# Kernel optimization log

Hardware: AMD Instinct MI355X
Metric: run time of the kernel (lower is better)

## Reference

```python
import jax, jax.numpy as jnp
import numpy as np

B, N, D, H = 4, 2048, 512, 8
KD = D // H  # per-head key/value dim = 64
NORM = 1.0 / np.sqrt(KD).astype(np.float32)


def setup_inputs() -> dict:
    key = jax.random.key(0)
    kq, km, k1, k2, k3 = jax.random.split(key, 5)
    s = 1.0 / np.sqrt(D)
    return {
        "queries": jax.random.normal(kq, (B, N, D), dtype=jnp.float32),
        "mask": jax.random.randint(km, (B, N, N), 0, 2).astype(jnp.bool_),
        "Wq": jax.random.normal(k1, (D, D), dtype=jnp.float32) * s,
        "Wk": jax.random.normal(k2, (D, D), dtype=jnp.float32) * s,
        "Wc": jax.random.normal(k3, (D, D), dtype=jnp.float32) * s,
    }


def reference(queries, mask, Wq, Wk, Wc):
    # Self-attention path (keys=None, values=None): V uses key_embed (Wk).
    Q = (queries @ Wq.T).reshape(B, N, H, KD)  # [B,N,H,kd]
    K = (queries @ Wk.T).reshape(B, N, H, KD)
    V = K  # original code: V = key_embed(queries) when values is None
    scores = NORM * jnp.einsum("bqhd,bkhd->bhqk", Q, K)  # [B,H,N,N]
    scores = jnp.where(mask[:, None, :, :], -jnp.inf, scores)
    attn = jax.nn.softmax(scores, axis=-1)
    out = jnp.einsum("bhqk,bkhd->bqhd", attn, V).reshape(B, N, H * KD)
    return out @ Wc.T  # [B,N,D]
```

## Files before the change

kernel.cpp:

```cpp
#include <hip/hip_runtime.h>
#include <hip/hip_bf16.h>
#include <math.h>

#define B_ 4
#define N_ 2048
#define D_ 512
#define H_ 8
#define NORM2_ 0.18033688011112042f

typedef __attribute__((ext_vector_type(8))) short short8;
typedef __attribute__((ext_vector_type(4))) float f32x4;
#define MFMA16(a, b, c) __builtin_amdgcn_mfma_f32_16x16x32_bf16(a, b, c, 0, 0, 0)
#define EXP2(x) __builtin_amdgcn_exp2f(x)

static __device__ __forceinline__ uint32_t pk2(float lo, float hi) {
  __hip_bfloat162 h = __float22bfloat162_rn(make_float2(lo, hi));
  return *(reinterpret_cast<uint32_t*>(&h));
}

static __device__ __forceinline__ void async16(const ushort* lds, const ushort* g) {
  __builtin_amdgcn_global_load_lds(
      (const __attribute__((address_space(1))) uint32_t*)g,
      (__attribute__((address_space(3))) uint32_t*)(ushort*)lds, 16, 0, 0);
}

__global__ __launch_bounds__(256) void prep(const float* __restrict__ q,
                                            const int* __restrict__ mask,
                                            const float* __restrict__ wq,
                                            const float* __restrict__ wk,
                                            const float* __restrict__ wc,
                                            ushort* __restrict__ Xb,
                                            ushort* __restrict__ Wb,
                                            uint32_t* __restrict__ pk) {
  const int bx = blockIdx.x;
  if (bx < 2048) {
    const int lane = threadIdx.x & 63;
    const int wid = ((bx << 8) + threadIdx.x) >> 6;
    for (int i = wid; i < 65536; i += 8192) {
      const int4 m = ((const int4*)mask)[(size_t)i * 64 + lane];
      uint32_t nib = (uint32_t)(m.x != 0) | ((uint32_t)(m.y != 0) << 1) |
                     ((uint32_t)(m.z != 0) << 2) | ((uint32_t)(m.w != 0) << 3);
      nib |= __shfl_xor(nib, 1) << 4;
      nib |= __shfl_xor(nib, 2) << 8;
      nib |= __shfl_xor(nib, 4) << 16;
      if ((lane & 7) == 0) pk[i * 8 + (lane >> 3)] = nib;
    }
  } else if (bx < 3072) {
    const int i = ((bx - 2048) << 8) + threadIdx.x;
    for (int j = i; j < 1048576; j += 262144) {
      const float4 v = ((const float4*)q)[j];
      uint2 o; o.x = pk2(v.x, v.y); o.y = pk2(v.z, v.w);
      ((uint2*)Xb)[j] = o;
    }
  } else {
    const int i = ((bx - 3072) << 8) + threadIdx.x;
    for (int j = i; j < 196608; j += 24576) {
      const int wi = j >> 16, off = j & 65535;
      const float* src = (wi == 0) ? wq : (wi == 1) ? wk : wc;
      const float4 v = ((const float4*)src)[off];
      uint2 o; o.x = pk2(v.x, v.y); o.y = pk2(v.z, v.w);
      ((uint2*)Wb)[j] = o;
    }
  }
}

__global__ __launch_bounds__(256) void merge(const ushort* __restrict__ P0,
                                             const float* __restrict__ l0,
                                             const float* __restrict__ l1,
                                             ushort* __restrict__ Ab) {
  const int j = (blockIdx.x << 8) + threadIdx.x;
  const int h = (j >> 3) & 7;
  const int tok = j >> 6;
  const int b = tok >> 11, n = tok & 2047;
  const int li = ((b * H_ + h) << 11) + n;
  const float inv = 1.f / (l0[li] + l1[li]);
  const uint4 a0 = ((const uint4*)P0)[j];
  const uint4 a1 = ((const uint4*)Ab)[j];
  uint4 o;
  const uint32_t* u0 = (const uint32_t*)&a0;
  const uint32_t* u1 = (const uint32_t*)&a1;
  uint32_t* uo = (uint32_t*)&o;
#pragma unroll
  for (int m = 0; m < 4; ++m) {
    const float lo = __uint_as_float(u0[m] << 16) + __uint_as_float(u1[m] << 16);
    const float hi = __uint_as_float(u0[m] & 0xFFFF0000u) +
                     __uint_as_float(u1[m] & 0xFFFF0000u);
    uo[m] = pk2(lo * inv, hi * inv);
  }
  ((uint4*)Ab)[j] = o;
}

template <int F32OUT>
__global__ __launch_bounds__(256) void gemm128(const ushort* __restrict__ X,
                                               const ushort* __restrict__ W0,
                                               const ushort* __restrict__ W1,
                                               void* __restrict__ C0,
                                               void* __restrict__ C1,
                                               float s0, float s1) {
  const ushort* Wp = (blockIdx.z == 0) ? W0 : W1;
  void* Cp = (blockIdx.z == 0) ? C0 : C1;
  const float sc = (blockIdx.z == 0) ? s0 : s1;
  const int t = threadIdx.x;
  const int w = t >> 6, lane = t & 63, quad = lane >> 4, c = lane & 15;
  const int wm = w & 1, wn = w >> 1;
  const int n0 = blockIdx.x * 128, m0 = blockIdx.y * 128;
  __shared__ __align__(16) ushort Xs[2][128][64];
  __shared__ __align__(16) ushort Ws[2][128][64];
  f32x4 acc[4][4];
#pragma unroll
  for (int i = 0; i < 4; ++i)
#pragma unroll
    for (int j = 0; j < 4; ++j) acc[i][j] = (f32x4){0.f, 0.f, 0.f, 0.f};

#define GSTAGE(bf, k0)                                                        \
  do {                                                                        \
    _Pragma("unroll") for (int g = 0; g < 4; ++g) {                           \
      const int id = w * 256 + g * 64 + lane;                                 \
      const int row = id >> 3, lch = id & 7;                                  \
      const int gch = lch ^ (row & 7);                                        \
      async16(&Xs[bf][row][lch * 8], X + (size_t)(m0 + row) * D_ + (k0) + gch * 8); \
      async16(&Ws[bf][row][lch * 8], Wp + (size_t)(n0 + row) * D_ + (k0) + gch * 8); \
    }                                                                         \
  } while (0)

  GSTAGE(0, 0);
  __syncthreads();
  const int NK = D_ / 64;
  for (int kt = 0; kt < NK; ++kt) {
    const int bf = kt & 1;
    if (kt + 1 < NK) GSTAGE(bf ^ 1, (kt + 1) * 64);
#pragma unroll
    for (int s = 0; s < 2; ++s) {
      short8 af[4], bt[4];
#pragma unroll
      for (int i = 0; i < 4; ++i) {
        const int rA = wn * 64 + i * 16 + c;
        af[i] = *(const short8*)&Ws[bf][rA][(((s * 4 + quad) ^ (rA & 7)) & 7) * 8];
        const int rB = wm * 64 + i * 16 + c;
        bt[i] = *(const short8*)&Xs[bf][rB][(((s * 4 + quad) ^ (rB & 7)) & 7) * 8];
      }
#pragma unroll
      for (int i = 0; i < 4; ++i)
#pragma unroll
        for (int j = 0; j < 4; ++j) acc[i][j] = MFMA16(af[i], bt[j], acc[i][j]);
    }
    if (kt + 1 < NK) __syncthreads();
  }
#undef GSTAGE
#pragma unroll
  for (int i = 0; i < 4; ++i)
#pragma unroll
    for (int j = 0; j < 4; ++j) {
      const size_t off =
          (size_t)(m0 + wm * 64 + j * 16 + c) * D_ + n0 + wn * 64 + i * 16 + quad * 4;
      if (F32OUT) {
        float4 v; v.x = acc[i][j][0]; v.y = acc[i][j][1]; v.z = acc[i][j][2]; v.w = acc[i][j][3];
        *(float4*)((float*)Cp + off) = v;
      } else {
        uint2 uv;
        uv.x = pk2(acc[i][j][0] * sc, acc[i][j][1] * sc);
        uv.y = pk2(acc[i][j][2] * sc, acc[i][j][3] * sc);
        *(uint2*)((ushort*)Cp + off) = uv;
      }
    }
}

__global__ __launch_bounds__(512) void attn_mfma(const ushort* __restrict__ Qb,
                                                 const ushort* __restrict__ Kb,
                                                 const uint32_t* __restrict__ pk,
                                                 ushort* __restrict__ P0,
                                                 ushort* __restrict__ P1,
                                                 float* __restrict__ l0,
                                                 float* __restrict__ l1) {
  const int qt128 = blockIdx.x >> 1, hf = blockIdx.x & 1;
  const int h = blockIdx.y, b = blockIdx.z;
  const int q0 = qt128 * 128;
  const int t = threadIdx.x;
  const int w = t >> 6, lane = t & 63, quad = lane >> 4, c = lane & 15;

  __shared__ __align__(16) ushort Ks[64][64];
  __shared__ __align__(16) uint32_t KtU[64][32];
  __shared__ __align__(16) ushort QP[8][16][72];
  ushort(*Qs)[64] = (ushort(*)[64]) & QP[0][0][0];
  ushort(*Pq)[16][72] = QP;

#pragma unroll
  for (int p = 0; p < 2; ++p) {
    const int id = t + p * 512;
    const int row = id >> 3, lch = id & 7, gch = lch ^ (row & 7);
    async16(&Qs[row][lch * 8], Qb + (size_t)(b * N_ + q0 + row) * D_ + h * 64 + gch * 8);
  }
  __syncthreads();
  const int rq = (w << 4) + c;
  const short8 bq0 = *(const short8*)&Qs[rq][((quad ^ (rq & 7)) & 7) * 8];
  const short8 bq1 = *(const short8*)&Qs[rq][(((4 + quad) ^ (rq & 7)) & 7) * 8];

  short8 vones;
#pragma unroll
  for (int i = 0; i < 8; ++i) vones[i] = (short)0x3F80;

  f32x4 o[4];
#pragma unroll
  for (int i = 0; i < 4; ++i) o[i] = (f32x4){0.f, 0.f, 0.f, 0.f};
  f32x4 o5 = (f32x4){0.f, 0.f, 0.f, 0.f};

  const int kp = t >> 3, ch = t & 7;
  const int r0 = 2 * kp, r1 = r0 + 1;
  const int ksw0 = ((ch ^ (r0 & 7)) & 7) * 8, ksw1 = ((ch ^ (r1 & 7)) & 7) * 8;
  const ushort* kb0 =
      Kb + (size_t)(b * N_ + hf * 1024 + 2 * kp) * D_ + h * 64 + ch * 8;
  const uint32_t* pkq =
      pk + ((size_t)(b * N_ + q0 + (w << 4) + c) << 6) + hf * 32;

  uint4 c0, c1;
  if (t < 256) {
    c0 = *(const uint4*)kb0;
    c1 = *(const uint4*)(kb0 + D_);
  }
  uint2 cm = *(const uint2*)pkq;
  uint4 nx0, nx1; uint2 nxm;

  const int NT = 16;
  for (int kt = 0; kt < NT; ++kt) {
    __syncthreads();
    if (t < 256) {
      *(uint4*)&Ks[r0][ksw0] = c0;
      *(uint4*)&Ks[r1][ksw1] = c1;
      const uint32_t* a0 = (const uint32_t*)&c0;
      const uint32_t* a1 = (const uint32_t*)&c1;
#pragma unroll
      for (int m = 0; m < 4; ++m) {
        const uint32_t lo = __builtin_amdgcn_perm(a1[m], a0[m], 0x05040100);
        const uint32_t hi = __builtin_amdgcn_perm(a1[m], a0[m], 0x07060302);
        const int j0 = 2 * m, j1 = 2 * m + 1;
        KtU[ch * 8 + j0][(kp & 3) | ((((kp >> 2) ^ j0 ^ ch) & 7) << 2)] = lo;
        KtU[ch * 8 + j1][(kp & 3) | ((((kp >> 2) ^ j1 ^ ch) & 7) << 2)] = hi;
      }
    }
    __syncthreads();

    if (kt + 1 < NT) {
      if (t < 256) {
        const ushort* kbn = kb0 + (size_t)(kt + 1) * 64 * D_;
        nx0 = *(const uint4*)kbn;
        nx1 = *(const uint4*)(kbn + D_);
      }
      nxm = *(const uint2*)(pkq + (kt + 1) * 2);
    }

#pragma unroll
    for (int tI = 0; tI < 4; ++tI) {
      const int rk = tI * 16 + c;
      const short8 aK0 = *(const short8*)&Ks[rk][((quad ^ (rk & 7)) & 7) * 8];
      const short8 aK1 = *(const short8*)&Ks[rk][(((4 + quad) ^ (rk & 7)) & 7) * 8];
      f32x4 z = (f32x4){0.f, 0.f, 0.f, 0.f};
      z = MFMA16(aK0, bq0, z);
      z = MFMA16(aK1, bq1, z);
      const uint32_t mw = (tI < 2) ? cm.x : cm.y;
      const int bb = ((tI & 1) << 4) + quad * 4;
      uint32_t pb[4];
#pragma unroll
      for (int r = 0; r < 4; ++r) {
        const float e = EXP2(z[r]);
        pb[r] = ((mw >> (bb + r)) & 1u) ? 0u : __float_as_uint(e);
      }
      const uint32_t pw0 = __builtin_amdgcn_perm(pb[1], pb[0], 0x07060302);
      const uint32_t pw1 = __builtin_amdgcn_perm(pb[3], pb[2], 0x07060302);
      *(uint2*)&Pq[w][c][tI * 16 + quad * 4] = make_uint2(pw0, pw1);
    }

    const short8 bp0 = *(const short8*)&Pq[w][c][quad * 8];
    const short8 bp1 = *(const short8*)&Pq[w][c][32 + quad * 8];
    o5 = MFMA16(vones, bp0, o5);
    o5 = MFMA16(vones, bp1, o5);
#pragma unroll
    for (int dt = 0; dt < 4; ++dt) {
      const int dd = dt * 16 + c;
      const int g = (c & 7) ^ ((2 * dt + (c >> 3)) & 7);
      const short8 aV0 = *(const short8*)&KtU[dd][((quad ^ g) & 7) << 2];
      const short8 aV1 = *(const short8*)&KtU[dd][(((4 + quad) ^ g) & 7) << 2];
      o[dt] = MFMA16(aV0, bp0, o[dt]);
      o[dt] = MFMA16(aV1, bp1, o[dt]);
    }

    if (kt + 1 < NT) {
      if (t < 256) { c0 = nx0; c1 = nx1; }
      cm = nxm;
    }
  }

  ushort* Pp = hf ? P1 : P0;
  float* lp = hf ? l1 : l0;
#pragma unroll
  for (int dt = 0; dt < 4; ++dt) {
    uint2 uv;
    uv.x = pk2(o[dt][0], o[dt][1]);
    uv.y = pk2(o[dt][2], o[dt][3]);
    *(uint2*)(Pp + (size_t)(b * N_ + q0 + (w << 4) + c) * D_ + h * 64 + dt * 16 + quad * 4) = uv;
  }
  if (quad == 0) lp[((b * H_ + h) << 11) + q0 + (w << 4) + c] = o5[0];
}

extern "C" void kernel_launch(void* const* d_in, const int* in_sizes, int n_in,
                              void* d_out, int out_size, void* d_ws, size_t ws_size,
                              hipStream_t stream) {
  const float* queries = (const float*)d_in[0];
  const int* mask = (const int*)d_in[1];
  const float* Wq = (const float*)d_in[2];
  const float* Wk = (const float*)d_in[3];
  const float* Wc = (const float*)d_in[4];
  float* out = (float*)d_out;

  const size_t nTok = (size_t)B_ * N_;
  const size_t nXD = nTok * D_;
  const size_t nW = (size_t)D_ * D_;
  ushort* Xb = (ushort*)d_ws;
  ushort* Wqb = Xb + nXD;
  ushort* Wkb = Wqb + nW;
  ushort* Wcb = Wkb + nW;
  ushort* Qb = Wcb + nW;
  ushort* Kb = Qb + nXD;
  ushort* Ab = Kb + nXD;
  uint32_t* pk = (uint32_t*)(Ab + nXD);
  ushort* P0 = Xb;
  ushort* P1 = Ab;
  float* l0 = (float*)Wqb;
  float* l1 = (float*)Wkb;

  prep<<<3168, 256, 0, stream>>>(queries, mask, Wq, Wk, Wc, Xb, Wqb, pk);
  gemm128<0><<<dim3(D_ / 128, (int)(nTok / 128), 2), 256, 0, stream>>>(
      Xb, Wqb, Wkb, Qb, Kb, NORM2_, 1.0f);
  attn_mfma<<<dim3(32, H_, B_), 512, 0, stream>>>(Qb, Kb, pk, P0, P1, l0, l1);
  merge<<<2048, 256, 0, stream>>>(P0, l0, l1, Ab);
  gemm128<1><<<dim3(D_ / 128, (int)(nTok / 128), 1), 256, 0, stream>>>(
      Ab, Wcb, nullptr, out, nullptr, 1.0f, 1.0f);
}
```

Baseline: 207.4 us.

## Fuse split-KV merge into output GEMM and use 512-thread GEMM blocks

Removes the separate merge kernel. The output projection GEMM now loads both partial attention outputs and the row sums, normalizes and sums them in registers, and writes the bf16 result into shared memory as its A operand. It also moves both GEMMs from 256 to 512 threads per block, with each wave computing a 64x32 tile instead of 64x64. This saves a kernel launch and a full round-trip of the merged activation through global memory. In exchange, the X operand is loaded synchronously into registers rather than by async copy, and each wave does less MFMA work per LDS load.

```diff
diff --git a/kernel.cpp b/kernel.cpp
--- a/kernel.cpp
+++ b/kernel.cpp
@@ -64,63 +64,36 @@
   }
 }
 
-__global__ __launch_bounds__(256) void merge(const ushort* __restrict__ P0,
-                                             const float* __restrict__ l0,
-                                             const float* __restrict__ l1,
-                                             ushort* __restrict__ Ab) {
-  const int j = (blockIdx.x << 8) + threadIdx.x;
-  const int h = (j >> 3) & 7;
-  const int tok = j >> 6;
-  const int b = tok >> 11, n = tok & 2047;
-  const int li = ((b * H_ + h) << 11) + n;
-  const float inv = 1.f / (l0[li] + l1[li]);
-  const uint4 a0 = ((const uint4*)P0)[j];
-  const uint4 a1 = ((const uint4*)Ab)[j];
-  uint4 o;
-  const uint32_t* u0 = (const uint32_t*)&a0;
-  const uint32_t* u1 = (const uint32_t*)&a1;
-  uint32_t* uo = (uint32_t*)&o;
-#pragma unroll
-  for (int m = 0; m < 4; ++m) {
-    const float lo = __uint_as_float(u0[m] << 16) + __uint_as_float(u1[m] << 16);
-    const float hi = __uint_as_float(u0[m] & 0xFFFF0000u) +
-                     __uint_as_float(u1[m] & 0xFFFF0000u);
-    uo[m] = pk2(lo * inv, hi * inv);
-  }
-  ((uint4*)Ab)[j] = o;
-}
-
-template <int F32OUT>
-__global__ __launch_bounds__(256) void gemm128(const ushort* __restrict__ X,
-                                               const ushort* __restrict__ W0,
-                                               const ushort* __restrict__ W1,
-                                               void* __restrict__ C0,
-                                               void* __restrict__ C1,
-                                               float s0, float s1) {
-  const ushort* Wp = (blockIdx.z == 0) ? W0 : W1;
-  void* Cp = (blockIdx.z == 0) ? C0 : C1;
-  const float sc = (blockIdx.z == 0) ? s0 : s1;
+__global__ __launch_bounds__(512) void gemmQK(const ushort* __restrict__ X,
+                                              const ushort* __restrict__ W0,
+                                              const ushort* __restrict__ W1,
+                                              ushort* __restrict__ C0,
+                                              ushort* __restrict__ C1,
+                                              float s0, float s1) {
+  const ushort* Wp = blockIdx.z ? W1 : W0;
+  ushort* Cp = blockIdx.z ? C1 : C0;
+  const float sc = blockIdx.z ? s1 : s0;
   const int t = threadIdx.x;
   const int w = t >> 6, lane = t & 63, quad = lane >> 4, c = lane & 15;
   const int wm = w & 1, wn = w >> 1;
   const int n0 = blockIdx.x * 128, m0 = blockIdx.y * 128;
   __shared__ __align__(16) ushort Xs[2][128][64];
   __shared__ __align__(16) ushort Ws[2][128][64];
-  f32x4 acc[4][4];
-#pragma unroll
-  for (int i = 0; i < 4; ++i)
+  f32x4 acc[2][4];
+#pragma unroll
+  for (int i = 0; i < 2; ++i)
 #pragma unroll
     for (int j = 0; j < 4; ++j) acc[i][j] = (f32x4){0.f, 0.f, 0.f, 0.f};
 
-#define GSTAGE(bf, k0)                                                        \
-  do {                                                                        \
-    _Pragma("unroll") for (int g = 0; g < 4; ++g) {                           \
-      const int id = w * 256 + g * 64 + lane;                                 \
-      const int row = id >> 3, lch = id & 7;                                  \
-      const int gch = lch ^ (row & 7);                                        \
+#define GSTAGE(bf, k0)                                                              \
+  do {                                                                              \
+    _Pragma("unroll") for (int p = 0; p < 2; ++p) {                                 \
+      const int id = t + p * 512;                                                   \
+      const int row = id >> 3, lch = id & 7;                                        \
+      const int gch = lch ^ (row & 7);                                              \
       async16(&Xs[bf][row][lch * 8], X + (size_t)(m0 + row) * D_ + (k0) + gch * 8); \
       async16(&Ws[bf][row][lch * 8], Wp + (size_t)(n0 + row) * D_ + (k0) + gch * 8); \
-    }                                                                         \
+    }                                                                               \
   } while (0)
 
   GSTAGE(0, 0);
@@ -131,16 +104,19 @@
     if (kt + 1 < NK) GSTAGE(bf ^ 1, (kt + 1) * 64);
 #pragma unroll
     for (int s = 0; s < 2; ++s) {
-      short8 af[4], bt[4];
-#pragma unroll
-      for (int i = 0; i < 4; ++i) {
-        const int rA = wn * 64 + i * 16 + c;
+      short8 af[2], bt[4];
+#pragma unroll
+      for (int i = 0; i < 2; ++i) {
+        const int rA = wn * 32 + i * 16 + c;
         af[i] = *(const short8*)&Ws[bf][rA][(((s * 4 + quad) ^ (rA & 7)) & 7) * 8];
-        const int rB = wm * 64 + i * 16 + c;
-        bt[i] = *(const short8*)&Xs[bf][rB][(((s * 4 + quad) ^ (rB & 7)) & 7) * 8];
-      }
-#pragma unroll
-      for (int i = 0; i < 4; ++i)
+      }
+#pragma unroll
+      for (int j = 0; j < 4; ++j) {
+        const int rB = wm * 64 + j * 16 + c;
+        bt[j] = *(const short8*)&Xs[bf][rB][(((s * 4 + quad) ^ (rB & 7)) & 7) * 8];
+      }
+#pragma unroll
+      for (int i = 0; i < 2; ++i)
 #pragma unroll
         for (int j = 0; j < 4; ++j) acc[i][j] = MFMA16(af[i], bt[j], acc[i][j]);
     }
@@ -148,20 +124,130 @@
   }
 #undef GSTAGE
 #pragma unroll
-  for (int i = 0; i < 4; ++i)
+  for (int i = 0; i < 2; ++i)
 #pragma unroll
     for (int j = 0; j < 4; ++j) {
       const size_t off =
-          (size_t)(m0 + wm * 64 + j * 16 + c) * D_ + n0 + wn * 64 + i * 16 + quad * 4;
-      if (F32OUT) {
-        float4 v; v.x = acc[i][j][0]; v.y = acc[i][j][1]; v.z = acc[i][j][2]; v.w = acc[i][j][3];
-        *(float4*)((float*)Cp + off) = v;
-      } else {
-        uint2 uv;
-        uv.x = pk2(acc[i][j][0] * sc, acc[i][j][1] * sc);
-        uv.y = pk2(acc[i][j][2] * sc, acc[i][j][3] * sc);
-        *(uint2*)((ushort*)Cp + off) = uv;
-      }
+          (size_t)(m0 + wm * 64 + j * 16 + c) * D_ + n0 + wn * 32 + i * 16 + quad * 4;
+      uint2 uv;
+      uv.x = pk2(acc[i][j][0] * sc, acc[i][j][1] * sc);
+      uv.y = pk2(acc[i][j][2] * sc, acc[i][j][3] * sc);
+      *(uint2*)(Cp + off) = uv;
+    }
+}
+
+__global__ __launch_bounds__(512) void gemmOut(const ushort* __restrict__ P0,
+                                               const ushort* __restrict__ P1,
+                                               const float* __restrict__ l0,
+                                               const float* __restrict__ l1,
+                                               const ushort* __restrict__ W,
+                                               float* __restrict__ out) {
+  const int t = threadIdx.x;
+  const int w = t >> 6, lane = t & 63, quad = lane >> 4, c = lane & 15;
+  const int wm = w & 1, wn = w >> 1;
+  const int n0 = blockIdx.x * 128, m0 = blockIdx.y * 128;
+  __shared__ __align__(16) ushort Xs[2][128][64];
+  __shared__ __align__(16) ushort Ws[2][128][64];
+  f32x4 acc[2][4];
+#pragma unroll
+  for (int i = 0; i < 2; ++i)
+#pragma unroll
+    for (int j = 0; j < 4; ++j) acc[i][j] = (f32x4){0.f, 0.f, 0.f, 0.f};
+
+  uint4 xa[2], xb[2];
+  float lsum[2];
+
+#define WSTAGE(bf, k0)                                                              \
+  do {                                                                              \
+    _Pragma("unroll") for (int p = 0; p < 2; ++p) {                                 \
+      const int id = t + p * 512;                                                   \
+      const int row = id >> 3, lch = id & 7;                                        \
+      const int gch = lch ^ (row & 7);                                              \
+      async16(&Ws[bf][row][lch * 8], W + (size_t)(n0 + row) * D_ + (k0) + gch * 8); \
+    }                                                                               \
+  } while (0)
+
+#define XLOAD(k0)                                                                   \
+  do {                                                                              \
+    _Pragma("unroll") for (int p = 0; p < 2; ++p) {                                 \
+      const int id = t + p * 512;                                                   \
+      const int row = id >> 3, lch = id & 7;                                        \
+      const int gch = lch ^ (row & 7);                                              \
+      const size_t j16 = (size_t)(m0 + row) * D_ + (k0) + gch * 8;                  \
+      xa[p] = *(const uint4*)(P0 + j16);                                            \
+      xb[p] = *(const uint4*)(P1 + j16);                                            \
+      const int tok = m0 + row;                                                     \
+      const int li = ((((tok >> 11) * H_) + ((k0) >> 6)) << 11) + (tok & 2047);     \
+      lsum[p] = l0[li] + l1[li];                                                    \
+    }                                                                               \
+  } while (0)
+
+#define XWRITE(bf)                                                                  \
+  do {                                                                              \
+    _Pragma("unroll") for (int p = 0; p < 2; ++p) {                                 \
+      const int id = t + p * 512;                                                   \
+      const int row = id >> 3, lch = id & 7;                                        \
+      const float inv = 1.f / lsum[p];                                              \
+      const uint32_t* u0 = (const uint32_t*)&xa[p];                                 \
+      const uint32_t* u1 = (const uint32_t*)&xb[p];                                 \
+      uint4 o;                                                                      \
+      uint32_t* uo = (uint32_t*)&o;                                                 \
+      _Pragma("unroll") for (int m = 0; m < 4; ++m) {                               \
+        const float lo = __uint_as_float(u0[m] << 16) + __uint_as_float(u1[m] << 16); \
+        const float hi = __uint_as_float(u0[m] & 0xFFFF0000u) +                     \
+                         __uint_as_float(u1[m] & 0xFFFF0000u);                      \
+        uo[m] = pk2(lo * inv, hi * inv);                                            \
+      }                                                                             \
+      *(uint4*)&Xs[bf][row][lch * 8] = o;                                           \
+    }                                                                               \
+  } while (0)
+
+  WSTAGE(0, 0);
+  XLOAD(0);
+  XWRITE(0);
+  __syncthreads();
+  const int NK = D_ / 64;
+  for (int kt = 0; kt < NK; ++kt) {
+    const int bf = kt & 1;
+    if (kt + 1 < NK) {
+      WSTAGE(bf ^ 1, (kt + 1) * 64);
+      XLOAD((kt + 1) * 64);
+    }
+#pragma unroll
+    for (int s = 0; s < 2; ++s) {
+      short8 af[2], bt[4];
+#pragma unroll
+      for (int i = 0; i < 2; ++i) {
+        const int rA = wn * 32 + i * 16 + c;
+        af[i] = *(const short8*)&Ws[bf][rA][(((s * 4 + quad) ^ (rA & 7)) & 7) * 8];
+      }
+#pragma unroll
+      for (int j = 0; j < 4; ++j) {
+        const int rB = wm * 64 + j * 16 + c;
+        bt[j] = *(const short8*)&Xs[bf][rB][(((s * 4 + quad) ^ (rB & 7)) & 7) * 8];
+      }
+#pragma unroll
+      for (int i = 0; i < 2; ++i)
+#pragma unroll
+        for (int j = 0; j < 4; ++j) acc[i][j] = MFMA16(af[i], bt[j], acc[i][j]);
+    }
+    if (kt + 1 < NK) {
+      XWRITE(bf ^ 1);
+      __syncthreads();
+    }
+  }
+#undef WSTAGE
+#undef XLOAD
+#undef XWRITE
+#pragma unroll
+  for (int i = 0; i < 2; ++i)
+#pragma unroll
+    for (int j = 0; j < 4; ++j) {
+      const size_t off =
+          (size_t)(m0 + wm * 64 + j * 16 + c) * D_ + n0 + wn * 32 + i * 16 + quad * 4;
+      float4 v;
+      v.x = acc[i][j][0]; v.y = acc[i][j][1]; v.z = acc[i][j][2]; v.w = acc[i][j][3];
+      *(float4*)(out + off) = v;
     }
 }
 
@@ -328,10 +414,9 @@
   float* l1 = (float*)Wkb;
 
   prep<<<3168, 256, 0, stream>>>(queries, mask, Wq, Wk, Wc, Xb, Wqb, pk);
-  gemm128<0><<<dim3(D_ / 128, (int)(nTok / 128), 2), 256, 0, stream>>>(
+  gemmQK<<<dim3(D_ / 128, (int)(nTok / 128), 2), 512, 0, stream>>>(
       Xb, Wqb, Wkb, Qb, Kb, NORM2_, 1.0f);
   attn_mfma<<<dim3(32, H_, B_), 512, 0, stream>>>(Qb, Kb, pk, P0, P1, l0, l1);
-  merge<<<2048, 256, 0, stream>>>(P0, l0, l1, Ab);
-  gemm128<1><<<dim3(D_ / 128, (int)(nTok / 128), 1), 256, 0, stream>>>(
-      Ab, Wcb, nullptr, out, nullptr, 1.0f, 1.0f);
-}
+  gemmOut<<<dim3(D_ / 128, (int)(nTok / 128)), 512, 0, stream>>>(
+      P0, P1, l0, l1, Wcb, out);
+}
```

Result: slower. 212.0 us (+2.2%).
